# Performance work log

Hardware: AMD Instinct MI355X
Metric: run time of the kernel (lower is better)

The kernel has to match this reference:

```python
import jax, jax.numpy as jnp
import numpy as np

N, E, G, H, D = 30000, 480000, 128, 4, 64
NF, EF, GF, L = 92, 50, 108, 5
EPS = 1e-3  # keras BatchNormalization default epsilon


def _bn(t, g, b, m, v):
    # inference-mode batch norm with running stats
    return (t - m) * jax.lax.rsqrt(v + EPS) * g + b


def _forward(x, edge_attr, global_features,
             node_W, node_b, edge_W, edge_b,
             conv_W, conv_att, conv_bias, conv_bn_g, conv_bn_b, conv_bn_m, conv_bn_v,
             ga_W0, ga_b0, ga_bn0_g, ga_bn0_b, ga_bn0_m, ga_bn0_v,
             ga_W1, ga_b1, ga_bn1_g, ga_bn1_b, ga_bn1_m, ga_bn1_v,
             ga_W2, ga_b2, out_W0, out_b0, out_W1, out_b1,
             edge_index, batch_idx, num_graphs):
    lrelu = lambda t: jax.nn.leaky_relu(t, 0.2)
    row, col = edge_index[0], edge_index[1]
    n = x.shape[0]

    x = lrelu(x @ node_W + node_b)          # [N, D] node embedding
    ea = lrelu(edge_attr @ edge_W + edge_b)  # [E, D] edge embedding

    def conv(xc, p):
        W, att, bias, g, b, m, v = p
        xi = (jnp.concatenate([xc[row], ea], -1) @ W).reshape(-1, H, D)  # [E,H,D]
        xj = (jnp.concatenate([xc[col], ea], -1) @ W).reshape(-1, H, D)
        score = jnp.einsum('ehd,hd->eh', jnp.concatenate([xi, xj], -1), att)
        a = jnp.exp(_bn(lrelu(score), g, b, m, v))            # [E,H]
        norm = jax.ops.segment_sum(a, row, num_segments=n)    # edge softmax denom
        a = a / norm[row]
        msg = xj * a[..., None]                               # [E,H,D]
        # faithful to original: transpose then flat reshape before scatter-add
        msg = jnp.transpose(msg, (1, 0, 2)).reshape(-1, H * D)
        agg = jax.ops.segment_sum(msg, row, num_segments=n)
        out = agg.reshape(n, H, D).mean(axis=1) + bias
        return xc + out, None  # residual connection (done in GATGNN.call)

    x, _ = jax.lax.scan(conv, x, (conv_W, conv_att, conv_bias,
                                  conv_bn_g, conv_bn_b, conv_bn_m, conv_bn_v))

    # global attention pooling
    feat = jnp.concatenate([x, global_features[batch_idx]], -1)  # [N, D+GF]
    h = jax.nn.relu(_bn(feat @ ga_W0 + ga_b0, ga_bn0_g, ga_bn0_b, ga_bn0_m, ga_bn0_v))
    h = jax.nn.relu(_bn(h @ ga_W1 + ga_b1, ga_bn1_g, ga_bn1_b, ga_bn1_m, ga_bn1_v))
    a = jnp.exp(h @ ga_W2 + ga_b2)                               # [N,1]
    norm = jax.ops.segment_sum(a, batch_idx, num_segments=num_graphs)
    a = a / norm[batch_idx]
    pooled = jax.ops.segment_sum(x * a, batch_idx, num_segments=num_graphs)  # [G,D]
    out = jax.nn.relu(pooled @ out_W0 + out_b0) @ out_W1 + out_b1
    return out.squeeze(-1)  # output_dim == 1


def setup_inputs() -> dict:
    key = jax.random.key(0)
    ks = jax.random.split(key, 16)
    s = 0.05
    return {
        'x': jax.random.normal(ks[0], (N, NF), jnp.float32),
        'edge_attr': jax.random.normal(ks[1], (E, EF), jnp.float32),
        'global_features': jax.random.normal(ks[2], (G, GF), jnp.float32),
        'node_W': jax.random.normal(ks[3], (NF, D)) * s, 'node_b': jnp.zeros((D,)),
        'edge_W': jax.random.normal(ks[4], (EF, D)) * s, 'edge_b': jnp.zeros((D,)),
        'conv_W': jax.random.normal(ks[5], (L, 2 * D, H * D)) * s,
        'conv_att': jax.random.normal(ks[6], (L, H, 2 * D)) * s,
        'conv_bias': jnp.zeros((L, D)),
        'conv_bn_g': jnp.ones((L, H)), 'conv_bn_b': jnp.zeros((L, H)),
        'conv_bn_m': jnp.zeros((L, H)), 'conv_bn_v': jnp.ones((L, H)),
        'ga_W0': jax.random.normal(ks[7], (D + GF, D)) * s, 'ga_b0': jnp.zeros((D,)),
        'ga_bn0_g': jnp.ones((D,)), 'ga_bn0_b': jnp.zeros((D,)),
        'ga_bn0_m': jnp.zeros((D,)), 'ga_bn0_v': jnp.ones((D,)),
        'ga_W1': jax.random.normal(ks[8], (D, D)) * s, 'ga_b1': jnp.zeros((D,)),
        'ga_bn1_g': jnp.ones((D,)), 'ga_bn1_b': jnp.zeros((D,)),
        'ga_bn1_m': jnp.zeros((D,)), 'ga_bn1_v': jnp.ones((D,)),
        'ga_W2': jax.random.normal(ks[9], (D, 1)) * s, 'ga_b2': jnp.zeros((1,)),
        'out_W0': jax.random.normal(ks[10], (D, D)) * s, 'out_b0': jnp.zeros((D,)),
        'out_W1': jax.random.normal(ks[11], (D, 1)) * s, 'out_b1': jnp.zeros((1,)),
        'edge_index': jax.random.randint(ks[12], (2, E), 0, N),
        'batch_idx': jnp.sort(jax.random.randint(ks[13], (N,), 0, G)),
        'num_graphs': G,
    }


def reference(x, edge_attr, global_features, node_W, node_b, edge_W, edge_b,
              conv_W, conv_att, conv_bias, conv_bn_g, conv_bn_b, conv_bn_m, conv_bn_v,
              ga_W0, ga_b0, ga_bn0_g, ga_bn0_b, ga_bn0_m, ga_bn0_v,
              ga_W1, ga_b1, ga_bn1_g, ga_bn1_b, ga_bn1_m, ga_bn1_v,
              ga_W2, ga_b2, out_W0, out_b0, out_W1, out_b1,
              edge_index, batch_idx, num_graphs):
    return _forward(x, edge_attr, global_features, node_W, node_b, edge_W, edge_b,
                    conv_W, conv_att, conv_bias, conv_bn_g, conv_bn_b, conv_bn_m, conv_bn_v,
                    ga_W0, ga_b0, ga_bn0_g, ga_bn0_b, ga_bn0_m, ga_bn0_v,
                    ga_W1, ga_b1, ga_bn1_g, ga_bn1_b, ga_bn1_m, ga_bn1_v,
                    ga_W2, ga_b2, out_W0, out_b0, out_W1, out_b1,
                    edge_index, batch_idx, num_graphs)
```

## Files before the change

### kernel.cpp

```cpp
#include <hip/hip_runtime.h>

constexpr int N = 30000, E = 480000, G = 128, H = 4, D = 64;
constexpr int NF = 92, EF = 50, GF = 108, L = 5;
constexpr int EQ = E / 4;
constexpr float EPS = 1e-3f;

__device__ __forceinline__ float lrelu(float t) { return t > 0.f ? t : 0.2f * t; }

__device__ __forceinline__ unsigned short f2bf(float f) {
  unsigned int u = __float_as_uint(f);
  u += 0x7FFFu + ((u >> 16) & 1u);
  return (unsigned short)(u >> 16);
}
__device__ __forceinline__ float bf2f(unsigned short s) {
  return __uint_as_float(((unsigned int)s) << 16);
}

__global__ __launch_bounds__(256) void hist_kernel(const int* __restrict__ row,
                                                   int* __restrict__ deg) {
  int e = blockIdx.x * 256 + threadIdx.x;
  atomicAdd(&deg[row[e]], 1);
}

__global__ __launch_bounds__(1024) void scan_kernel(const int* __restrict__ deg,
                                                    int* __restrict__ start) {
  __shared__ int wsum[16];
  __shared__ int cbase;
  if (threadIdx.x == 0) cbase = 0;
  __syncthreads();
  int lane = threadIdx.x & 63, wave = threadIdx.x >> 6;
  for (int base = 0; base < N; base += 1024) {
    int i = base + (int)threadIdx.x;
    int v = (i < N) ? deg[i] : 0;
    int s = v;
#pragma unroll
    for (int off = 1; off < 64; off <<= 1) { int t = __shfl_up(s, off); if (lane >= off) s += t; }
    if (lane == 63) wsum[wave] = s;
    __syncthreads();
    if (wave == 0 && lane < 16) {
      int w = wsum[lane];
#pragma unroll
      for (int off = 1; off < 16; off <<= 1) { int t = __shfl_up(w, off); if (lane >= off) w += t; }
      wsum[lane] = w;
    }
    __syncthreads();
    int wbase = wave ? wsum[wave - 1] : 0;
    if (i < N) start[i] = cbase + wbase + (s - v);
    __syncthreads();
    if (threadIdx.x == 0) cbase += wsum[15];
    __syncthreads();
  }
  if (threadIdx.x == 0) start[N] = cbase;
}

__global__ __launch_bounds__(256) void fill_kernel(
    const int* __restrict__ row, const int* __restrict__ start, int* __restrict__ cur,
    int* __restrict__ eid_s) {
  int e = blockIdx.x * 256 + threadIdx.x;
  int r = row[e];
  int pos = start[r] + atomicAdd(&cur[r], 1);
  eid_s[pos] = e;
}

__global__ __launch_bounds__(256) void gbound_kernel(const int* __restrict__ batch,
                                                     int* __restrict__ gstart) {
  int n = blockIdx.x * 256 + threadIdx.x;
  if (n >= N) return;
  int b = batch[n];
  int prev = (n == 0) ? -1 : batch[n - 1];
  for (int g = prev + 1; g <= b; g++) gstart[g] = n;
  if (n == N - 1) for (int g = b + 1; g <= G; g++) gstart[g] = N;
}

template <int K, bool BF16OUT>
__global__ __launch_bounds__(256) void embed7_kernel(
    const float* __restrict__ in, const float* __restrict__ W,
    const float* __restrict__ bias, float* __restrict__ outF,
    unsigned short* __restrict__ outB, int ntiles) {
  constexpr int KP = (K + 3) & ~3;
  constexpr int NL = (16 * K + 255) / 256;
  __shared__ float xs[2][16][KP];
  int tid = threadIdx.x, lane = tid & 63, wave = tid >> 6;
  if (K != KP) {
    for (int f = tid; f < 2 * 16 * KP; f += 256)
      if (f % KP >= K) ((float*)xs)[f] = 0.f;
  }
  float wreg[KP];
#pragma unroll
  for (int k = 0; k < K; k++) wreg[k] = W[k * 64 + lane];
#pragma unroll
  for (int k = K; k < KP; k++) wreg[k] = 0.f;
  float bb = bias[lane];
  float stage[NL];
  int t = blockIdx.x;
  if (t < ntiles) {
#pragma unroll
    for (int i = 0; i < NL; i++) { int f = tid + i * 256; if (f < 16 * K) stage[i] = in[(size_t)t * 16 * K + f]; }
#pragma unroll
    for (int i = 0; i < NL; i++) { int f = tid + i * 256; if (f < 16 * K) xs[0][f / K][f % K] = stage[i]; }
  }
  __syncthreads();
  int cur = 0;
  for (; t < ntiles; t += gridDim.x) {
    int nxt = t + gridDim.x;
    if (nxt < ntiles) {
#pragma unroll
      for (int i = 0; i < NL; i++) { int f = tid + i * 256; if (f < 16 * K) stage[i] = in[(size_t)nxt * 16 * K + f]; }
    }
    float a0 = 0.f, a1 = 0.f, a2 = 0.f, a3 = 0.f;
#pragma unroll
    for (int kc = 0; kc < KP / 4; kc++) {
      float4 x0 = *(const float4*)&xs[cur][wave * 4 + 0][kc * 4];
      float4 x1 = *(const float4*)&xs[cur][wave * 4 + 1][kc * 4];
      float4 x2 = *(const float4*)&xs[cur][wave * 4 + 2][kc * 4];
      float4 x3 = *(const float4*)&xs[cur][wave * 4 + 3][kc * 4];
      float w0 = wreg[kc * 4], w1 = wreg[kc * 4 + 1], w2 = wreg[kc * 4 + 2], w3 = wreg[kc * 4 + 3];
      a0 = fmaf(x0.x, w0, fmaf(x0.y, w1, fmaf(x0.z, w2, fmaf(x0.w, w3, a0))));
      a1 = fmaf(x1.x, w0, fmaf(x1.y, w1, fmaf(x1.z, w2, fmaf(x1.w, w3, a1))));
      a2 = fmaf(x2.x, w0, fmaf(x2.y, w1, fmaf(x2.z, w2, fmaf(x2.w, w3, a2))));
      a3 = fmaf(x3.x, w0, fmaf(x3.y, w1, fmaf(x3.z, w2, fmaf(x3.w, w3, a3))));
    }
    size_t o = ((size_t)t * 16 + wave * 4) * 64 + lane;
    float r0 = lrelu(a0 + bb), r1 = lrelu(a1 + bb), r2 = lrelu(a2 + bb), r3 = lrelu(a3 + bb);
    if (BF16OUT) {
      outB[o] = f2bf(r0); outB[o + 64] = f2bf(r1);
      outB[o + 128] = f2bf(r2); outB[o + 192] = f2bf(r3);
    } else {
      outF[o] = r0; outF[o + 64] = r1; outF[o + 128] = r2; outF[o + 192] = r3;
    }
    if (nxt < ntiles) {
#pragma unroll
      for (int i = 0; i < NL; i++) { int f = tid + i * 256; if (f < 16 * K) xs[cur ^ 1][f / K][f % K] = stage[i]; }
    }
    __syncthreads();
    cur ^= 1;
  }
}

__global__ __launch_bounds__(256) void aes_watt_all_kernel(
    const float* __restrict__ conv_W, const float* __restrict__ conv_att,
    float* __restrict__ AesT, float* __restrict__ WattT) {
  int l = blockIdx.x;
  const float* W = conv_W + (size_t)l * 128 * 256;
  const float* att = conv_att + (size_t)l * H * 128;
  int t = threadIdx.x;
  {
    int h = t >> 6, k = t & 63;
    float acc = 0.f;
    for (int d = 0; d < 64; d++)
      acc = fmaf(W[(64 + k) * 256 + h * 64 + d], att[h * 128 + d] + att[h * 128 + 64 + d], acc);
    AesT[l * 256 + h * 64 + k] = acc;
  }
  for (int idx = t; idx < 512; idx += 256) {
    int hh = idx >> 6, k = idx & 63;
    int h = hh >> 1, ij = hh & 1;
    float acc = 0.f;
    for (int d = 0; d < 64; d++)
      acc = fmaf(W[k * 256 + h * 64 + d], att[h * 128 + ij * 64 + d], acc);
    WattT[l * 512 + idx] = acc;
  }
}

constexpr int QS_CPL = 960;
__global__ __launch_bounds__(256) void qs3_kernel(
    const unsigned short* __restrict__ ea, const float* __restrict__ AesT,
    float* __restrict__ qsAll) {
  int l = blockIdx.x / QS_CPL;
  int bx = blockIdx.x % QS_CPL;
  int tid = threadIdx.x;
  int k16 = tid & 3;
  float A[4][16];
#pragma unroll
  for (int h = 0; h < 4; h++) {
    const float* Ap = &AesT[l * 256 + h * 64 + k16 * 16];
#pragma unroll
    for (int j4 = 0; j4 < 4; j4++) {
      float4 v = ((const float4*)Ap)[j4];
      A[h][4 * j4] = v.x; A[h][4 * j4 + 1] = v.y;
      A[h][4 * j4 + 2] = v.z; A[h][4 * j4 + 3] = v.w;
    }
  }
  float* qOut = qsAll + (size_t)l * E * 4;
  for (int c = bx; c < E / 64; c += QS_CPL) {
    int e = c * 64 + (tid >> 2);
    const uint4* base = (const uint4*)&ea[(size_t)e * 64 + k16 * 16];
    uint4 ra = base[0], rb = base[1];
    float xv[16];
    {
      unsigned int uu[8] = {ra.x, ra.y, ra.z, ra.w, rb.x, rb.y, rb.z, rb.w};
#pragma unroll
      for (int i = 0; i < 8; i++) {
        xv[2 * i]     = __uint_as_float(uu[i] << 16);
        xv[2 * i + 1] = __uint_as_float(uu[i] & 0xFFFF0000u);
      }
    }
    float q0 = 0.f, q1 = 0.f, q2 = 0.f, q3 = 0.f;
#pragma unroll
    for (int j = 0; j < 16; j++) {
      float x = xv[j];
      q0 = fmaf(x, A[0][j], q0);
      q1 = fmaf(x, A[1][j], q1);
      q2 = fmaf(x, A[2][j], q2);
      q3 = fmaf(x, A[3][j], q3);
    }
    q0 += __shfl_xor(q0, 1); q1 += __shfl_xor(q1, 1);
    q2 += __shfl_xor(q2, 2 - 1); q3 += __shfl_xor(q3, 1);
    q0 += __shfl_xor(q0, 2); q1 += __shfl_xor(q1, 2);
    q2 += __shfl_xor(q2, 2); q3 += __shfl_xor(q3, 2);
    float qv = (k16 == 0) ? q0 : (k16 == 1) ? q1 : (k16 == 2) ? q2 : q3;
    qOut[(size_t)e * 4 + k16] = qv;
  }
}

__global__ __launch_bounds__(256) void xw_kernel(
    const float* __restrict__ xc, const float* __restrict__ W, const float* __restrict__ WattT,
    unsigned short* __restrict__ xWh, float* __restrict__ pi, float* __restrict__ pj) {
  __shared__ float xs[16][64];
  __shared__ float wlT[8][68];
  int tid = threadIdx.x, blk = blockIdx.x, n0 = blk * 16;
  for (int f = tid; f < 1024; f += 256) xs[f >> 6][f & 63] = xc[(size_t)n0 * 64 + f];
  for (int f = tid; f < 512; f += 256) wlT[f >> 6][f & 63] = WattT[f];
  __syncthreads();
  float acc[16];
#pragma unroll
  for (int n = 0; n < 16; n++) acc[n] = 0.f;
#pragma unroll 4
  for (int kc = 0; kc < 16; kc++) {
    float w0 = W[(4 * kc + 0) * 256 + tid];
    float w1 = W[(4 * kc + 1) * 256 + tid];
    float w2 = W[(4 * kc + 2) * 256 + tid];
    float w3 = W[(4 * kc + 3) * 256 + tid];
#pragma unroll
    for (int n = 0; n < 16; n++) {
      float4 xv = *(const float4*)&xs[n][4 * kc];
      acc[n] = fmaf(xv.x, w0, fmaf(xv.y, w1, fmaf(xv.z, w2, fmaf(xv.w, w3, acc[n]))));
    }
  }
  int h = tid >> 6, dd = tid & 63;
#pragma unroll
  for (int n = 0; n < 16; n++)
    xWh[((size_t)h * N + (n0 + n)) * 64 + dd] = f2bf(acc[n]);
  if (tid < 128) {
    int n = tid >> 3, hh = tid & 7;
    float a = 0.f;
#pragma unroll
    for (int kc = 0; kc < 16; kc++) {
      float4 xv = *(const float4*)&xs[n][4 * kc];
      float4 wv = *(const float4*)&wlT[hh][4 * kc];
      a = fmaf(xv.x, wv.x, fmaf(xv.y, wv.y, fmaf(xv.z, wv.z, fmaf(xv.w, wv.w, a))));
    }
    int hq = hh >> 1, ij = hh & 1;
    float* dst = ij ? pj : pi;
    dst[(n0 + n) * 4 + hq] = a;
  }
}

__global__ __launch_bounds__(256) void score2_kernel(
    const float* __restrict__ qs, const float* __restrict__ pi, const float* __restrict__ pj,
    const int* __restrict__ row, const int* __restrict__ col,
    const float* __restrict__ bng, const float* __restrict__ bnb,
    const float* __restrict__ bnm, const float* __restrict__ bnv,
    float* __restrict__ aArr) {
  int e = blockIdx.x * 256 + threadIdx.x;
  int r = row[e], c = col[e];
  float4 q = ((const float4*)qs)[e];
  float4 piv = ((const float4*)pi)[r];
  float4 pjv = ((const float4*)pj)[c];
  float A0 = bng[0] * rsqrtf(bnv[0] + EPS), B0 = bnb[0] - bnm[0] * A0;
  float A1 = bng[1] * rsqrtf(bnv[1] + EPS), B1 = bnb[1] - bnm[1] * A1;
  float A2 = bng[2] * rsqrtf(bnv[2] + EPS), B2 = bnb[2] - bnm[2] * A2;
  float A3 = bng[3] * rsqrtf(bnv[3] + EPS), B3 = bnb[3] - bnm[3] * A3;
  float4 out;
  out.x = expf(lrelu(piv.x + pjv.x + q.x) * A0 + B0);
  out.y = expf(lrelu(piv.y + pjv.y + q.y) * A1 + B1);
  out.z = expf(lrelu(piv.z + pjv.z + q.z) * A2 + B2);
  out.w = expf(lrelu(piv.w + pjv.w + q.w) * A3 + B3);
  ((float4*)aArr)[e] = out;
}

__global__ __launch_bounds__(256) void normsum_kernel(
    const float* __restrict__ aArr, const int* __restrict__ start,
    const int* __restrict__ eid_s, float* __restrict__ inv) {
  int n = blockIdx.x * 256 + threadIdx.x;
  if (n >= N) return;
  int s0 = start[n], s1 = start[n + 1];
  float4 s = {0.f, 0.f, 0.f, 0.f};
  int p = s0;
  for (; p + 4 <= s1; p += 4) {
    int e0 = eid_s[p], e1 = eid_s[p + 1], e2 = eid_s[p + 2], e3 = eid_s[p + 3];
    float4 a0 = ((const float4*)aArr)[e0];
    float4 a1 = ((const float4*)aArr)[e1];
    float4 a2 = ((const float4*)aArr)[e2];
    float4 a3 = ((const float4*)aArr)[e3];
    s.x += (a0.x + a1.x) + (a2.x + a3.x);
    s.y += (a0.y + a1.y) + (a2.y + a3.y);
    s.z += (a0.z + a1.z) + (a2.z + a3.z);
    s.w += (a0.w + a1.w) + (a2.w + a3.w);
  }
  for (; p < s1; p++) {
    float4 a = ((const float4*)aArr)[eid_s[p]];
    s.x += a.x; s.y += a.y; s.z += a.z; s.w += a.w;
  }
  float4 iv;
  if (s1 > s0) { iv.x = 1.f / s.x; iv.y = 1.f / s.y; iv.z = 1.f / s.z; iv.w = 1.f / s.w; }
  else         { iv.x = iv.y = iv.z = iv.w = 0.f; }
  ((float4*)inv)[n] = iv;
}

__global__ __launch_bounds__(256) void zyquad_kernel(
    const float* __restrict__ aArr, const float* __restrict__ invA,
    const unsigned short* __restrict__ ea, const unsigned short* __restrict__ xWh,
    const int* __restrict__ row, const int* __restrict__ col,
    unsigned short* __restrict__ ZYbf) {
  int q = blockIdx.x * 4 + (threadIdx.x >> 6);
  int lane = threadIdx.x & 63;
  const unsigned short* er = ea + (size_t)q * 256 + lane;
  float e0 = bf2f(er[0]), e1 = bf2f(er[64]), e2 = bf2f(er[128]), e3 = bf2f(er[192]);
  int4 rw = *(const int4*)&row[4 * q];
  int4 cl = *(const int4*)&col[4 * q];
  float4 A0 = ((const float4*)aArr)[4 * q + 0];
  float4 A1 = ((const float4*)aArr)[4 * q + 1];
  float4 A2 = ((const float4*)aArr)[4 * q + 2];
  float4 A3 = ((const float4*)aArr)[4 * q + 3];
  float4 I0 = ((const float4*)invA)[rw.x];
  float4 I1 = ((const float4*)invA)[rw.y];
  float4 I2 = ((const float4*)invA)[rw.z];
  float4 I3 = ((const float4*)invA)[rw.w];
  float c0[4] = {A0.x * I0.x, A0.y * I0.y, A0.z * I0.z, A0.w * I0.w};
  float c1[4] = {A1.x * I1.x, A1.y * I1.y, A1.z * I1.z, A1.w * I1.w};
  float c2[4] = {A2.x * I2.x, A2.y * I2.y, A2.z * I2.z, A2.w * I2.w};
  float c3[4] = {A3.x * I3.x, A3.y * I3.y, A3.z * I3.z, A3.w * I3.w};
#pragma unroll
  for (int h = 0; h < 4; h++) {
    const unsigned short* xw = xWh + (size_t)h * N * 64 + lane;
    float g0 = bf2f(xw[(size_t)cl.x * 64]);
    float g1 = bf2f(xw[(size_t)cl.y * 64]);
    float g2 = bf2f(xw[(size_t)cl.z * 64]);
    float g3 = bf2f(xw[(size_t)cl.w * 64]);
    float y = fmaf(c0[h], e0, fmaf(c1[h], e1, fmaf(c2[h], e2, c3[h] * e3)));
    float z = fmaf(c0[h], g0, fmaf(c1[h], g1, fmaf(c2[h], g2, c3[h] * g3)));
    size_t r = (size_t)h * EQ + q;
    ZYbf[r * 128 + lane] = f2bf(z);
    ZYbf[r * 128 + 64 + lane] = f2bf(y);
  }
}

__global__ __launch_bounds__(256) void scatter2_kernel(
    const unsigned short* __restrict__ ZYbf,
    const int* __restrict__ start, const int* __restrict__ eid_s,
    float* __restrict__ out1, float* __restrict__ Bacc) {
  int wave = threadIdx.x >> 6, lane = threadIdx.x & 63;
  int n = blockIdx.x * 4 + wave;
  int s0 = __builtin_amdgcn_readfirstlane(start[n]);
  int s1 = __builtin_amdgcn_readfirstlane(start[n + 1]);
  float m = 0.f;
  float b0 = 0.f, b1 = 0.f, b2 = 0.f, b3 = 0.f;
  int p = s0;
  for (; p + 4 <= s1; p += 4) {
    int r0 = eid_s[p], r1 = eid_s[p + 1], r2 = eid_s[p + 2], r3 = eid_s[p + 3];
    float z0 = bf2f(ZYbf[(size_t)r0 * 128 + lane]);
    float z1 = bf2f(ZYbf[(size_t)r1 * 128 + lane]);
    float z2 = bf2f(ZYbf[(size_t)r2 * 128 + lane]);
    float z3 = bf2f(ZYbf[(size_t)r3 * 128 + lane]);
    float y0 = bf2f(ZYbf[(size_t)r0 * 128 + 64 + lane]);
    float y1 = bf2f(ZYbf[(size_t)r1 * 128 + 64 + lane]);
    float y2 = bf2f(ZYbf[(size_t)r2 * 128 + 64 + lane]);
    float y3 = bf2f(ZYbf[(size_t)r3 * 128 + 64 + lane]);
    m += (z0 + z1) + (z2 + z3);
    int h0 = r0 / EQ, h1 = r1 / EQ, h2 = r2 / EQ, h3 = r3 / EQ;
    if (h0 == 0) b0 += y0; else if (h0 == 1) b1 += y0; else if (h0 == 2) b2 += y0; else b3 += y0;
    if (h1 == 0) b0 += y1; else if (h1 == 1) b1 += y1; else if (h1 == 2) b2 += y1; else b3 += y1;
    if (h2 == 0) b0 += y2; else if (h2 == 1) b1 += y2; else if (h2 == 2) b2 += y2; else b3 += y2;
    if (h3 == 0) b0 += y3; else if (h3 == 1) b1 += y3; else if (h3 == 2) b2 += y3; else b3 += y3;
  }
  for (; p < s1; p++) {
    int r = eid_s[p];
    float z = bf2f(ZYbf[(size_t)r * 128 + lane]);
    float y = bf2f(ZYbf[(size_t)r * 128 + 64 + lane]);
    m += z;
    int h = r / EQ;
    if (h == 0) b0 += y; else if (h == 1) b1 += y; else if (h == 2) b2 += y; else b3 += y;
  }
  out1[(size_t)n * 64 + lane] = m;
  float* Bn = Bacc + (size_t)n * 256 + lane;
  Bn[0] = b0; Bn[64] = b1; Bn[128] = b2; Bn[192] = b3;
}

__global__ __launch_bounds__(256) void finish_kernel(
    const float* __restrict__ out1, const float* __restrict__ Bacc,
    const float* __restrict__ W, const float* __restrict__ bias, float* __restrict__ xc) {
  __shared__ float Bl[16][256];
  int tid = threadIdx.x, blk = blockIdx.x;
  for (int f = tid; f < 4096; f += 256) Bl[f >> 8][f & 255] = Bacc[(size_t)blk * 4096 + f];
  __syncthreads();
  int lane = tid & 63, wave = tid >> 6;
  float a0 = 0.f, a1 = 0.f, a2 = 0.f, a3 = 0.f;
#pragma unroll
  for (int h = 0; h < 4; h++) {
#pragma unroll 4
    for (int kc = 0; kc < 16; kc++) {
      float w0 = W[(64 + 4 * kc + 0) * 256 + h * 64 + lane];
      float w1 = W[(64 + 4 * kc + 1) * 256 + h * 64 + lane];
      float w2 = W[(64 + 4 * kc + 2) * 256 + h * 64 + lane];
      float w3 = W[(64 + 4 * kc + 3) * 256 + h * 64 + lane];
      float4 b0v = *(const float4*)&Bl[wave * 4 + 0][h * 64 + 4 * kc];
      float4 b1v = *(const float4*)&Bl[wave * 4 + 1][h * 64 + 4 * kc];
      float4 b2v = *(const float4*)&Bl[wave * 4 + 2][h * 64 + 4 * kc];
      float4 b3v = *(const float4*)&Bl[wave * 4 + 3][h * 64 + 4 * kc];
      a0 = fmaf(b0v.x, w0, fmaf(b0v.y, w1, fmaf(b0v.z, w2, fmaf(b0v.w, w3, a0))));
      a1 = fmaf(b1v.x, w0, fmaf(b1v.y, w1, fmaf(b1v.z, w2, fmaf(b1v.w, w3, a1))));
      a2 = fmaf(b2v.x, w0, fmaf(b2v.y, w1, fmaf(b2v.z, w2, fmaf(b2v.w, w3, a2))));
      a3 = fmaf(b3v.x, w0, fmaf(b3v.y, w1, fmaf(b3v.z, w2, fmaf(b3v.w, w3, a3))));
    }
  }
  float bb = bias[lane];
  size_t i0 = (size_t)(blk * 16 + wave * 4) * 64 + lane;
  xc[i0]       += bb + 0.25f * (out1[i0] + a0);
  xc[i0 + 64]  += bb + 0.25f * (out1[i0 + 64] + a1);
  xc[i0 + 128] += bb + 0.25f * (out1[i0 + 128] + a2);
  xc[i0 + 192] += bb + 0.25f * (out1[i0 + 192] + a3);
}

__global__ __launch_bounds__(256) void gacontrib_kernel(
    const float* __restrict__ gfeat, const float* __restrict__ W0,
    const float* __restrict__ b0, float* __restrict__ gc) {
  __shared__ float gs[16][GF];
  int tid = threadIdx.x, blk = blockIdx.x;
  int lane = tid & 63, wave = tid >> 6;
  for (int f = tid; f < 16 * GF; f += 256) gs[f / GF][f % GF] = gfeat[(size_t)blk * 16 * GF + f];
  float wreg[GF];
#pragma unroll
  for (int k = 0; k < GF; k++) wreg[k] = W0[(64 + k) * 64 + lane];
  __syncthreads();
  float a0 = 0.f, a1 = 0.f, a2 = 0.f, a3 = 0.f;
#pragma unroll
  for (int kc = 0; kc < GF / 4; kc++) {
    float4 x0 = *(const float4*)&gs[wave * 4 + 0][kc * 4];
    float4 x1 = *(const float4*)&gs[wave * 4 + 1][kc * 4];
    float4 x2 = *(const float4*)&gs[wave * 4 + 2][kc * 4];
    float4 x3 = *(const float4*)&gs[wave * 4 + 3][kc * 4];
    float w0 = wreg[kc * 4], w1 = wreg[kc * 4 + 1], w2 = wreg[kc * 4 + 2], w3 = wreg[kc * 4 + 3];
    a0 = fmaf(x0.x, w0, fmaf(x0.y, w1, fmaf(x0.z, w2, fmaf(x0.w, w3, a0))));
    a1 = fmaf(x1.x, w0, fmaf(x1.y, w1, fmaf(x1.z, w2, fmaf(x1.w, w3, a1))));
    a2 = fmaf(x2.x, w0, fmaf(x2.y, w1, fmaf(x2.z, w2, fmaf(x2.w, w3, a2))));
    a3 = fmaf(x3.x, w0, fmaf(x3.y, w1, fmaf(x3.z, w2, fmaf(x3.w, w3, a3))));
  }
  float bb = b0[lane];
  size_t o = ((size_t)blk * 16 + wave * 4) * 64 + lane;
  gc[o]       = a0 + bb;
  gc[o + 64]  = a1 + bb;
  gc[o + 128] = a2 + bb;
  gc[o + 192] = a3 + bb;
}

__global__ __launch_bounds__(256) void ga0_kernel(
    const float* __restrict__ xc, const float* __restrict__ gc, const int* __restrict__ batch,
    const float* __restrict__ W0,
    const float* __restrict__ g0, const float* __restrict__ bb0,
    const float* __restrict__ m0, const float* __restrict__ v0,
    float* __restrict__ hout, int ntiles) {
  __shared__ float xs[16][64];
  __shared__ int bl[16];
  int tid = threadIdx.x, lane = tid & 63, wave = tid >> 6;
  float wreg[64];
#pragma unroll
  for (int k = 0; k < 64; k++) wreg[k] = W0[k * 64 + lane];
  float sc = rsqrtf(v0[lane] + EPS) * g0[lane];
  float mm = m0[lane], be = bb0[lane];
  for (int t = blockIdx.x; t < ntiles; t += gridDim.x) {
    __syncthreads();
    if (tid < 16) bl[tid] = batch[t * 16 + tid];
    for (int f = tid; f < 1024; f += 256) xs[f >> 6][f & 63] = xc[(size_t)t * 1024 + f];
    __syncthreads();
    float a0 = 0.f, a1 = 0.f, a2 = 0.f, a3 = 0.f;
#pragma unroll
    for (int kc = 0; kc < 16; kc++) {
      float4 x0 = *(const float4*)&xs[wave * 4 + 0][kc * 4];
      float4 x1 = *(const float4*)&xs[wave * 4 + 1][kc * 4];
      float4 x2 = *(const float4*)&xs[wave * 4 + 2][kc * 4];
      float4 x3 = *(const float4*)&xs[wave * 4 + 3][kc * 4];
      float w0 = wreg[kc * 4], w1 = wreg[kc * 4 + 1], w2 = wreg[kc * 4 + 2], w3 = wreg[kc * 4 + 3];
      a0 = fmaf(x0.x, w0, fmaf(x0.y, w1, fmaf(x0.z, w2, fmaf(x0.w, w3, a0))));
      a1 = fmaf(x1.x, w0, fmaf(x1.y, w1, fmaf(x1.z, w2, fmaf(x1.w, w3, a1))));
      a2 = fmaf(x2.x, w0, fmaf(x2.y, w1, fmaf(x2.z, w2, fmaf(x2.w, w3, a2))));
      a3 = fmaf(x3.x, w0, fmaf(x3.y, w1, fmaf(x3.z, w2, fmaf(x3.w, w3, a3))));
    }
    a0 += gc[(size_t)bl[wave * 4 + 0] * 64 + lane];
    a1 += gc[(size_t)bl[wave * 4 + 1] * 64 + lane];
    a2 += gc[(size_t)bl[wave * 4 + 2] * 64 + lane];
    a3 += gc[(size_t)bl[wave * 4 + 3] * 64 + lane];
    size_t o = ((size_t)t * 16 + wave * 4) * 64 + lane;
    hout[o]       = fmaxf((a0 - mm) * sc + be, 0.f);
    hout[o + 64]  = fmaxf((a1 - mm) * sc + be, 0.f);
    hout[o + 128] = fmaxf((a2 - mm) * sc + be, 0.f);
    hout[o + 192] = fmaxf((a3 - mm) * sc + be, 0.f);
  }
}

__global__ __launch_bounds__(256) void ga1_kernel(
    const float* __restrict__ hbuf,
    const float* __restrict__ W1, const float* __restrict__ b1,
    const float* __restrict__ g1, const float* __restrict__ bb1,
    const float* __restrict__ m1, const float* __restrict__ v1,
    const float* __restrict__ W2, const float* __restrict__ b2,
    float* __restrict__ a_un, int ntiles) {
  __shared__ float hsh[16][64];
  int tid = threadIdx.x, lane = tid & 63, wave = tid >> 6;
  float wreg[64];
#pragma unroll
  for (int k = 0; k < 64; k++) wreg[k] = W1[k * 64 + lane];
  float sc1 = rsqrtf(v1[lane] + EPS) * g1[lane];
  float mm1 = m1[lane], be1 = bb1[lane], bb1v = b1[lane];
  float w2v = W2[lane], b2v = b2[0];
  for (int t = blockIdx.x; t < ntiles; t += gridDim.x) {
    __syncthreads();
    for (int f = tid; f < 1024; f += 256) hsh[f >> 6][f & 63] = hbuf[(size_t)t * 1024 + f];
    __syncthreads();
    float c0 = 0.f, c1 = 0.f, c2 = 0.f, c3 = 0.f;
#pragma unroll
    for (int kc = 0; kc < 16; kc++) {
      float4 x0 = *(const float4*)&hsh[wave * 4 + 0][kc * 4];
      float4 x1 = *(const float4*)&hsh[wave * 4 + 1][kc * 4];
      float4 x2 = *(const float4*)&hsh[wave * 4 + 2][kc * 4];
      float4 x3 = *(const float4*)&hsh[wave * 4 + 3][kc * 4];
      float w0 = wreg[kc * 4], w1 = wreg[kc * 4 + 1], w2 = wreg[kc * 4 + 2], w3 = wreg[kc * 4 + 3];
      c0 = fmaf(x0.x, w0, fmaf(x0.y, w1, fmaf(x0.z, w2, fmaf(x0.w, w3, c0))));
      c1 = fmaf(x1.x, w0, fmaf(x1.y, w1, fmaf(x1.z, w2, fmaf(x1.w, w3, c1))));
      c2 = fmaf(x2.x, w0, fmaf(x2.y, w1, fmaf(x2.z, w2, fmaf(x2.w, w3, c2))));
      c3 = fmaf(x3.x, w0, fmaf(x3.y, w1, fmaf(x3.z, w2, fmaf(x3.w, w3, c3))));
    }
    float p0 = fmaxf((c0 + bb1v - mm1) * sc1 + be1, 0.f) * w2v;
    float p1 = fmaxf((c1 + bb1v - mm1) * sc1 + be1, 0.f) * w2v;
    float p2 = fmaxf((c2 + bb1v - mm1) * sc1 + be1, 0.f) * w2v;
    float p3 = fmaxf((c3 + bb1v - mm1) * sc1 + be1, 0.f) * w2v;
#pragma unroll
    for (int off = 1; off < 64; off <<= 1) {
      p0 += __shfl_xor(p0, off); p1 += __shfl_xor(p1, off);
      p2 += __shfl_xor(p2, off); p3 += __shfl_xor(p3, off);
    }
    if (lane < 4) {
      float pv = (lane == 0) ? p0 : (lane == 1) ? p1 : (lane == 2) ? p2 : p3;
      a_un[t * 16 + wave * 4 + lane] = expf(pv + b2v);
    }
  }
}

__global__ __launch_bounds__(256) void pool2_kernel(
    const float* __restrict__ xc, const float* __restrict__ a_un,
    const int* __restrict__ gstart, float* __restrict__ pooled) {
  __shared__ float red[4][64];
  __shared__ float s_norm;
  int g = blockIdx.x;
  int tid = threadIdx.x, lane = tid & 63, wave = tid >> 6;
  int s0 = gstart[g], s1 = gstart[g + 1];
  float ns = 0.f;
  for (int n = s0 + tid; n < s1; n += 256) ns += a_un[n];
#pragma unroll
  for (int off = 1; off < 64; off <<= 1) ns += __shfl_xor(ns, off);
  if (lane == 0) red[wave][0] = ns;
  __syncthreads();
  if (tid == 0) s_norm = (red[0][0] + red[1][0]) + (red[2][0] + red[3][0]);
  __syncthreads();
  float inv = (s1 > s0) ? 1.f / s_norm : 0.f;
  __syncthreads();
  float acc = 0.f;
  for (int n = s0 + wave; n < s1; n += 4)
    acc = fmaf(xc[(size_t)n * 64 + lane], a_un[n], acc);
  red[wave][lane] = acc;
  __syncthreads();
  if (wave == 0)
    pooled[(size_t)g * 64 + lane] =
        inv * ((red[0][lane] + red[1][lane]) + (red[2][lane] + red[3][lane]));
}

__global__ __launch_bounds__(256) void final_kernel(
    const float* __restrict__ pooled, const float* __restrict__ W0,
    const float* __restrict__ b0, const float* __restrict__ W1,
    const float* __restrict__ b1, float* __restrict__ out) {
  int g = blockIdx.x * 4 + (threadIdx.x >> 6);
  int d = threadIdx.x & 63;
  float pv = pooled[g * 64 + d];
  float acc = b0[d];
  for (int k = 0; k < 64; k++) acc = fmaf(__shfl(pv, k), W0[k * 64 + d], acc);
  acc = fmaxf(acc, 0.f);
  float p = acc * W1[d];
  for (int off = 1; off < 64; off <<= 1) p += __shfl_xor(p, off);
  if (d == 0) out[g] = p + b1[0];
}

extern "C" void kernel_launch(void* const* d_in, const int* in_sizes, int n_in,
                              void* d_out, int out_size, void* d_ws, size_t ws_size,
                              hipStream_t stream) {
  (void)in_sizes; (void)n_in; (void)out_size; (void)ws_size;
  const float* x_in    = (const float*)d_in[0];
  const float* ea_in   = (const float*)d_in[1];
  const float* gf      = (const float*)d_in[2];
  const float* node_W  = (const float*)d_in[3];
  const float* node_b  = (const float*)d_in[4];
  const float* edge_W  = (const float*)d_in[5];
  const float* edge_b  = (const float*)d_in[6];
  const float* conv_W  = (const float*)d_in[7];
  const float* conv_att= (const float*)d_in[8];
  const float* conv_bias=(const float*)d_in[9];
  const float* bn_g = (const float*)d_in[10];
  const float* bn_b = (const float*)d_in[11];
  const float* bn_m = (const float*)d_in[12];
  const float* bn_v = (const float*)d_in[13];
  const float* ga_W0 = (const float*)d_in[14]; const float* ga_b0 = (const float*)d_in[15];
  const float* ga0g = (const float*)d_in[16];  const float* ga0b = (const float*)d_in[17];
  const float* ga0m = (const float*)d_in[18];  const float* ga0v = (const float*)d_in[19];
  const float* ga_W1 = (const float*)d_in[20]; const float* ga_b1 = (const float*)d_in[21];
  const float* ga1g = (const float*)d_in[22];  const float* ga1b = (const float*)d_in[23];
  const float* ga1m = (const float*)d_in[24];  const float* ga1v = (const float*)d_in[25];
  const float* ga_W2 = (const float*)d_in[26]; const float* ga_b2 = (const float*)d_in[27];
  const float* out_W0 = (const float*)d_in[28]; const float* out_b0 = (const float*)d_in[29];
  const float* out_W1 = (const float*)d_in[30]; const float* out_b1 = (const float*)d_in[31];
  const int* eidx  = (const int*)d_in[32];
  const int* row   = eidx;
  const int* col   = eidx + E;
  const int* batch = (const int*)d_in[33];

  float* ws = (float*)d_ws;
  size_t off = 0;
  auto alloc = [&](size_t n) { float* p = ws + off; off += (n + 63) & ~(size_t)63; return p; };
  float* x_cur  = alloc((size_t)N * D);
  unsigned short* ea_bf = (unsigned short*)alloc((size_t)E * 32);
  unsigned short* xWh   = (unsigned short*)alloc((size_t)N * 128);
  unsigned short* ZYbf  = (unsigned short*)alloc((size_t)E * 64);
  float* pi     = alloc((size_t)N * 4);
  float* pj     = alloc((size_t)N * 4);
  float* aArr   = alloc((size_t)E * 4);
  float* invA   = alloc((size_t)N * 4);
  float* out1   = alloc((size_t)N * 64);
  float* Bacc   = alloc((size_t)N * 256);
  float* AesT   = alloc(L * 256);
  float* WattT  = alloc(L * 512);
  float* a_un   = alloc(N);
  float* pooled = alloc((size_t)G * 64);
  int* start = (int*)alloc(N + 1);
  int* gstart = (int*)alloc(G + 1);
  int* eid_s = (int*)alloc(E);
  float* qsAll  = alloc((size_t)L * E * 4);
  int* deg = (int*)xWh;
  int* cur = deg + N;
  float* gcontrib = (float*)xWh;
  float* hbuf     = Bacc;

  hipMemsetAsync(deg, 0, (size_t)2 * N * sizeof(int), stream);
  hist_kernel<<<E / 256, 256, 0, stream>>>(row, deg);
  scan_kernel<<<1, 1024, 0, stream>>>(deg, start);
  fill_kernel<<<E / 256, 256, 0, stream>>>(row, start, cur, eid_s);
  gbound_kernel<<<(N + 255) / 256, 256, 0, stream>>>(batch, gstart);

  embed7_kernel<NF, false><<<960, 256, 0, stream>>>(x_in, node_W, node_b, x_cur, nullptr, N / 16);
  embed7_kernel<EF, true><<<1920, 256, 0, stream>>>(ea_in, edge_W, edge_b, nullptr, ea_bf, E / 16);

  aes_watt_all_kernel<<<L, 256, 0, stream>>>(conv_W, conv_att, AesT, WattT);
  qs3_kernel<<<L * QS_CPL, 256, 0, stream>>>(ea_bf, AesT, qsAll);

  for (int l = 0; l < L; l++) {
    const float* W = conv_W + (size_t)l * 128 * 256;
    xw_kernel<<<N / 16, 256, 0, stream>>>(x_cur, W, WattT + l * 512, xWh, pi, pj);
    score2_kernel<<<E / 256, 256, 0, stream>>>(qsAll + (size_t)l * E * 4, pi, pj, row, col,
                                               bn_g + l * H, bn_b + l * H,
                                               bn_m + l * H, bn_v + l * H, aArr);
    normsum_kernel<<<(N + 255) / 256, 256, 0, stream>>>(aArr, start, eid_s, invA);
    zyquad_kernel<<<EQ / 4, 256, 0, stream>>>(aArr, invA, ea_bf, xWh, row, col, ZYbf);
    scatter2_kernel<<<N / 4, 256, 0, stream>>>(ZYbf, start, eid_s, out1, Bacc);
    finish_kernel<<<N / 16, 256, 0, stream>>>(out1, Bacc, W, conv_bias + l * D, x_cur);
  }

  gacontrib_kernel<<<G / 16, 256, 0, stream>>>(gf, ga_W0, ga_b0, gcontrib);
  ga0_kernel<<<960, 256, 0, stream>>>(x_cur, gcontrib, batch, ga_W0,
                                      ga0g, ga0b, ga0m, ga0v, hbuf, N / 16);
  ga1_kernel<<<960, 256, 0, stream>>>(hbuf, ga_W1, ga_b1,
                                      ga1g, ga1b, ga1m, ga1v, ga_W2, ga_b2,
                                      a_un, N / 16);
  pool2_kernel<<<G, 256, 0, stream>>>(x_cur, a_un, gstart, pooled);
  final_kernel<<<G / 4, 256, 0, stream>>>(pooled, out_W0, out_b0, out_W1, out_b1,
                                          (float*)d_out);
}
```

Measured before the change: 1.211 ms.

## Write ZY rows in CSR-sorted order so the scatter reads contiguously

Setup now records each edge's sorted position and a per-position byte holding the head index. The zyquad kernel writes each Z/Y row straight to its CSR-sorted slot. The scatter kernel can then stream rows contiguously for each node, with no eid_s indirection and no integer divide. This moves the random access from the scatter's reads to zyquad's writes, and it adds a one-time setup kernel plus extra buffers.

Measured after the change: 1.234 ms. About the same (+1.9%).

```diff
diff --git a/kernel.cpp b/kernel.cpp
--- a/kernel.cpp
+++ b/kernel.cpp
@@ -55,11 +55,18 @@
 
 __global__ __launch_bounds__(256) void fill_kernel(
     const int* __restrict__ row, const int* __restrict__ start, int* __restrict__ cur,
-    int* __restrict__ eid_s) {
+    int* __restrict__ eid_s, int* __restrict__ spos) {
   int e = blockIdx.x * 256 + threadIdx.x;
   int r = row[e];
   int pos = start[r] + atomicAdd(&cur[r], 1);
   eid_s[pos] = e;
+  spos[e] = pos;
+}
+
+__global__ __launch_bounds__(256) void hs8_kernel(const int* __restrict__ eid_s,
+                                                  unsigned char* __restrict__ hs8) {
+  int p = blockIdx.x * 256 + threadIdx.x;
+  if (p < E) hs8[p] = (unsigned char)(eid_s[p] / EQ);
 }
 
 __global__ __launch_bounds__(256) void gbound_kernel(const int* __restrict__ batch,
@@ -204,7 +211,7 @@
       q3 = fmaf(x, A[3][j], q3);
     }
     q0 += __shfl_xor(q0, 1); q1 += __shfl_xor(q1, 1);
-    q2 += __shfl_xor(q2, 2 - 1); q3 += __shfl_xor(q3, 1);
+    q2 += __shfl_xor(q2, 1); q3 += __shfl_xor(q3, 1);
     q0 += __shfl_xor(q0, 2); q1 += __shfl_xor(q1, 2);
     q2 += __shfl_xor(q2, 2); q3 += __shfl_xor(q3, 2);
     float qv = (k16 == 0) ? q0 : (k16 == 1) ? q1 : (k16 == 2) ? q2 : q3;
@@ -311,7 +318,7 @@
     const float* __restrict__ aArr, const float* __restrict__ invA,
     const unsigned short* __restrict__ ea, const unsigned short* __restrict__ xWh,
     const int* __restrict__ row, const int* __restrict__ col,
-    unsigned short* __restrict__ ZYbf) {
+    const int* __restrict__ spos, unsigned short* __restrict__ ZYperm) {
   int q = blockIdx.x * 4 + (threadIdx.x >> 6);
   int lane = threadIdx.x & 63;
   const unsigned short* er = ea + (size_t)q * 256 + lane;
@@ -339,15 +346,15 @@
     float g3 = bf2f(xw[(size_t)cl.w * 64]);
     float y = fmaf(c0[h], e0, fmaf(c1[h], e1, fmaf(c2[h], e2, c3[h] * e3)));
     float z = fmaf(c0[h], g0, fmaf(c1[h], g1, fmaf(c2[h], g2, c3[h] * g3)));
-    size_t r = (size_t)h * EQ + q;
-    ZYbf[r * 128 + lane] = f2bf(z);
-    ZYbf[r * 128 + 64 + lane] = f2bf(y);
-  }
-}
-
-__global__ __launch_bounds__(256) void scatter2_kernel(
-    const unsigned short* __restrict__ ZYbf,
-    const int* __restrict__ start, const int* __restrict__ eid_s,
+    size_t p = (size_t)spos[h * EQ + q];
+    ZYperm[p * 128 + lane] = f2bf(z);
+    ZYperm[p * 128 + 64 + lane] = f2bf(y);
+  }
+}
+
+__global__ __launch_bounds__(256) void scatter3_kernel(
+    const unsigned short* __restrict__ ZYperm, const unsigned char* __restrict__ hs8,
+    const int* __restrict__ start,
     float* __restrict__ out1, float* __restrict__ Bacc) {
   int wave = threadIdx.x >> 6, lane = threadIdx.x & 63;
   int n = blockIdx.x * 4 + wave;
@@ -357,28 +364,23 @@
   float b0 = 0.f, b1 = 0.f, b2 = 0.f, b3 = 0.f;
   int p = s0;
   for (; p + 4 <= s1; p += 4) {
-    int r0 = eid_s[p], r1 = eid_s[p + 1], r2 = eid_s[p + 2], r3 = eid_s[p + 3];
-    float z0 = bf2f(ZYbf[(size_t)r0 * 128 + lane]);
-    float z1 = bf2f(ZYbf[(size_t)r1 * 128 + lane]);
-    float z2 = bf2f(ZYbf[(size_t)r2 * 128 + lane]);
-    float z3 = bf2f(ZYbf[(size_t)r3 * 128 + lane]);
-    float y0 = bf2f(ZYbf[(size_t)r0 * 128 + 64 + lane]);
-    float y1 = bf2f(ZYbf[(size_t)r1 * 128 + 64 + lane]);
-    float y2 = bf2f(ZYbf[(size_t)r2 * 128 + 64 + lane]);
-    float y3 = bf2f(ZYbf[(size_t)r3 * 128 + 64 + lane]);
+    const unsigned short* zy = ZYperm + (size_t)p * 128;
+    float z0 = bf2f(zy[lane]),        y0 = bf2f(zy[64 + lane]);
+    float z1 = bf2f(zy[128 + lane]),  y1 = bf2f(zy[192 + lane]);
+    float z2 = bf2f(zy[256 + lane]),  y2 = bf2f(zy[320 + lane]);
+    float z3 = bf2f(zy[384 + lane]),  y3 = bf2f(zy[448 + lane]);
+    int h0 = hs8[p], h1 = hs8[p + 1], h2 = hs8[p + 2], h3 = hs8[p + 3];
     m += (z0 + z1) + (z2 + z3);
-    int h0 = r0 / EQ, h1 = r1 / EQ, h2 = r2 / EQ, h3 = r3 / EQ;
     if (h0 == 0) b0 += y0; else if (h0 == 1) b1 += y0; else if (h0 == 2) b2 += y0; else b3 += y0;
     if (h1 == 0) b0 += y1; else if (h1 == 1) b1 += y1; else if (h1 == 2) b2 += y1; else b3 += y1;
     if (h2 == 0) b0 += y2; else if (h2 == 1) b1 += y2; else if (h2 == 2) b2 += y2; else b3 += y2;
     if (h3 == 0) b0 += y3; else if (h3 == 1) b1 += y3; else if (h3 == 2) b2 += y3; else b3 += y3;
   }
   for (; p < s1; p++) {
-    int r = eid_s[p];
-    float z = bf2f(ZYbf[(size_t)r * 128 + lane]);
-    float y = bf2f(ZYbf[(size_t)r * 128 + 64 + lane]);
+    const unsigned short* zy = ZYperm + (size_t)p * 128;
+    float z = bf2f(zy[lane]), y = bf2f(zy[64 + lane]);
     m += z;
-    int h = r / EQ;
+    int h = hs8[p];
     if (h == 0) b0 += y; else if (h == 1) b1 += y; else if (h == 2) b2 += y; else b3 += y;
   }
   out1[(size_t)n * 64 + lane] = m;
@@ -626,7 +628,7 @@
   float* x_cur  = alloc((size_t)N * D);
   unsigned short* ea_bf = (unsigned short*)alloc((size_t)E * 32);
   unsigned short* xWh   = (unsigned short*)alloc((size_t)N * 128);
-  unsigned short* ZYbf  = (unsigned short*)alloc((size_t)E * 64);
+  unsigned short* ZYperm= (unsigned short*)alloc((size_t)E * 64);
   float* pi     = alloc((size_t)N * 4);
   float* pj     = alloc((size_t)N * 4);
   float* aArr   = alloc((size_t)E * 4);
@@ -640,6 +642,8 @@
   int* start = (int*)alloc(N + 1);
   int* gstart = (int*)alloc(G + 1);
   int* eid_s = (int*)alloc(E);
+  int* spos  = (int*)alloc(E);
+  unsigned char* hs8 = (unsigned char*)alloc(E / 4 + 64);
   float* qsAll  = alloc((size_t)L * E * 4);
   int* deg = (int*)xWh;
   int* cur = deg + N;
@@ -649,7 +653,8 @@
   hipMemsetAsync(deg, 0, (size_t)2 * N * sizeof(int), stream);
   hist_kernel<<<E / 256, 256, 0, stream>>>(row, deg);
   scan_kernel<<<1, 1024, 0, stream>>>(deg, start);
-  fill_kernel<<<E / 256, 256, 0, stream>>>(row, start, cur, eid_s);
+  fill_kernel<<<E / 256, 256, 0, stream>>>(row, start, cur, eid_s, spos);
+  hs8_kernel<<<(E + 255) / 256, 256, 0, stream>>>(eid_s, hs8);
   gbound_kernel<<<(N + 255) / 256, 256, 0, stream>>>(batch, gstart);
 
   embed7_kernel<NF, false><<<960, 256, 0, stream>>>(x_in, node_W, node_b, x_cur, nullptr, N / 16);
@@ -665,8 +670,8 @@
                                                bn_g + l * H, bn_b + l * H,
                                                bn_m + l * H, bn_v + l * H, aArr);
     normsum_kernel<<<(N + 255) / 256, 256, 0, stream>>>(aArr, start, eid_s, invA);
-    zyquad_kernel<<<EQ / 4, 256, 0, stream>>>(aArr, invA, ea_bf, xWh, row, col, ZYbf);
-    scatter2_kernel<<<N / 4, 256, 0, stream>>>(ZYbf, start, eid_s, out1, Bacc);
+    zyquad_kernel<<<EQ / 4, 256, 0, stream>>>(aArr, invA, ea_bf, xWh, row, col, spos, ZYperm);
+    scatter3_kernel<<<N / 4, 256, 0, stream>>>(ZYperm, hs8, start, out1, Bacc);
     finish_kernel<<<N / 16, 256, 0, stream>>>(out1, Bacc, W, conv_bias + l * D, x_cur);
   }
 
```
